# Optimization experiments

Hardware: AMD Instinct MI355X
Metric: run time of the kernel (lower is better)

## Reference

```python
import jax, jax.numpy as jnp
import numpy as np

B, N, C, K = 4, 1024, 384, 10


def _sqdist(a, b):
    # a: [B,P,3], b: [B,M,3] -> [B,P,M] squared euclidean distance
    d = (jnp.sum(a * a, -1)[:, :, None] + jnp.sum(b * b, -1)[:, None, :]
         - 2.0 * jnp.einsum('bpc,bmc->bpm', a, b))
    return jnp.maximum(d, 0.0)


def _gather(points, idx):
    # points: [B,M,C], idx: [B,...] int -> [B,...,C]  (index_points)
    return jax.vmap(lambda p, i: p[i])(points, idx)


def setup_inputs() -> dict:
    key = jax.random.key(0)
    ks = jax.random.split(key, 8)
    def lin(k_, fan_in, fan_out):
        return jax.random.normal(k_, (fan_in, fan_out), jnp.float32) * (1.0 / np.sqrt(fan_in))
    return {
        'q': jax.random.normal(ks[0], (B, N, C), jnp.float32),
        'q_pos': jax.random.normal(ks[1], (B, N, 3), jnp.float32),
        'Wv': lin(ks[2], C, C), 'bv': jnp.zeros((C,), jnp.float32),
        'W1': lin(ks[3], 2 * C, C), 'b1': jnp.zeros((C,), jnp.float32),
        'ln_g': jnp.ones((C,), jnp.float32), 'ln_b': jnp.zeros((C,), jnp.float32),
        'W2': lin(ks[4], C, 3),
        'Wk': lin(ks[5], 2 * C, C), 'bk': jnp.zeros((C,), jnp.float32),
    }


def reference(q, q_pos, Wv, bv, W1, b1, ln_g, ln_b, W2, Wk, bk):
    Bq, Nq, Cq = q.shape
    # 1) KNN of each query among all points (self-attn: v=q, v_pos=q_pos)
    d = _sqdist(q_pos, q_pos)                      # [B,N,N]
    _, idx = jax.lax.top_k(-d, K)                  # [B,N,K] (smallest distances)
    # 2) offset prediction from gathered projected features + query feature
    v_off = q @ Wv + bv                            # [B,N,C]
    off_local_v = _gather(v_off, idx)              # [B,N,K,C]
    qk = jnp.broadcast_to(q[:, :, None, :], (Bq, Nq, K, Cq))
    shift_feat = jnp.concatenate([off_local_v, qk], -1)  # [B,N,K,2C]
    h = shift_feat @ W1 + b1
    mu = jnp.mean(h, -1, keepdims=True)
    var = jnp.var(h, -1, keepdims=True)
    h = (h - mu) / jnp.sqrt(var + 1e-5) * ln_g + ln_b     # LayerNorm
    h = jax.nn.gelu(h, approximate=False)
    offset = jnp.tanh(h @ W2)                      # [B,N,K,3]
    # 3) deformed positions, scaled by half the local bbox extent
    local_v_pos = _gather(q_pos, idx)              # [B,N,K,3]
    scale = (local_v_pos.max(-2) - local_v_pos.min(-2))[:, :, None, :] * 0.5
    shift_pos = (local_v_pos + offset * scale).reshape(Bq, Nq * K, 3)
    # 4) three_nn + three_interpolate (inverse-squared-distance weights)
    d2 = _sqdist(shift_pos, q_pos)                 # [B,NK,N]
    negd, idx3 = jax.lax.top_k(-d2, 3)             # [B,NK,3]
    dist = -negd
    w = 1.0 / (dist + 1e-8)
    w = w / jnp.sum(w, -1, keepdims=True)
    feats3 = _gather(q, idx3)                      # [B,NK,3,C]
    interp = jnp.einsum('bpt,bptc->bpc', w, feats3).reshape(Bq, Nq, K, Cq)
    # 5) graph conv: concat(diff, q) -> Linear -> LeakyReLU(0.2) -> max over K
    feature = jnp.concatenate([interp - qk, qk], -1)      # [B,N,K,2C]
    out = jax.nn.leaky_relu(feature @ Wk + bk, negative_slope=0.2)
    return out.max(-2)                             # [B,N,C]
```

## Files before the change

### kernel.cpp

```cpp
#include <hip/hip_runtime.h>
#include <math.h>

#define BB 4
#define NN 1024
#define CC 384
#define KK 10
#define NKK (NN*KK)

typedef __attribute__((ext_vector_type(8))) short short8v;
typedef __attribute__((ext_vector_type(8))) unsigned short ushort8v;
typedef __attribute__((ext_vector_type(4))) float f32x4;

template <int NA>
__device__ __forceinline__ void wave_sum_arr(float* a) {
  #pragma unroll
  for (int off = 32; off > 0; off >>= 1) {
    float t[NA];
    #pragma unroll
    for (int u = 0; u < NA; ++u) t[u] = __shfl_xor(a[u], off, 64);
    #pragma unroll
    for (int u = 0; u < NA; ++u) a[u] += t[u];
  }
}

__device__ __forceinline__ unsigned short f2bf(float x) {
  unsigned int b = __float_as_uint(x);
  return (unsigned short)((b + 0x7fffu + ((b >> 16) & 1u)) >> 16);
}
__device__ __forceinline__ float bf2f(unsigned short h) {
  return __uint_as_float(((unsigned int)h) << 16);
}

#define NB_CVT  (BB * NN * CC / 1024)
#define NB_PB   (2 * CC * CC / 256)
#define NB_PREP (NB_CVT + NB_PB + 3)
__global__ __launch_bounds__(256) void prep_gemm_kernel(
    const float* __restrict__ q,
    const float* __restrict__ W1, const float* __restrict__ b1,
    const float* __restrict__ bv, const float* __restrict__ bk,
    const float* __restrict__ Wk, const float* __restrict__ Wv,
    unsigned short* __restrict__ qh, unsigned short* __restrict__ ql,
    unsigned short* __restrict__ Wt,
    float* __restrict__ bias_uv, float* __restrict__ bias_pb,
    float* __restrict__ M1p) {
  int blk = blockIdx.x;
  int tid = threadIdx.x;
  if (blk < NB_CVT) {
    int i = (blk * 256 + tid) * 4;
    float4 v = *reinterpret_cast<const float4*>(q + i);
    float x[4] = {v.x, v.y, v.z, v.w};
    #pragma unroll
    for (int j = 0; j < 4; ++j) {
      unsigned short h = f2bf(x[j]);
      qh[i + j] = h;
      ql[i + j] = f2bf(x[j] - bf2f(h));
    }
    return;
  }
  if (blk < NB_CVT + NB_PB) {
    int idx = (blk - NB_CVT) * 256 + tid;
    int n = idx / CC, k = idx % CC;
    float v;
    if (n < CC) v = Wk[(size_t)k * CC + n];
    else        v = Wk[(size_t)CC * CC + k * CC + (n - CC)] - Wk[(size_t)k * CC + (n - CC)];
    Wt[(size_t)n * CC + k] = f2bf(v);
    return;
  }
  if (blk < NB_PREP) {
    int j = (blk - NB_CVT - NB_PB) * 256 + tid;
    if (j >= 2 * CC) return;
    if (j < CC) { bias_uv[j] = 0.f; bias_pb[j] = 0.f; }
    else {
      int c = j - CC;
      float s = b1[c];
      for (int i = 0; i < CC; ++i) s += bv[i] * W1[i * CC + c];
      bias_uv[j] = s;
      bias_pb[j] = bk[c];
    }
    return;
  }
  {
    int r = blk - NB_PREP;
    int bx = r % 3, by = (r / 3) % 3, bz = r / 9;
    __shared__ float As[16][132];
    __shared__ float Bs[16][128];
    int tx = tid & 15, ty = tid >> 4;
    int row0 = by * 128, col0 = bx * 128;
    int k0 = bz * 48;
    float acc[8][8] = {};
    int arow = tid >> 2, akc = (tid & 3) << 2;
    int brow = tid >> 5, bcol = (tid & 31) << 2;
    for (int kt = k0; kt < k0 + 48; kt += 16) {
      #pragma unroll
      for (int h = 0; h < 2; ++h) {
        int rr = arow + 64 * h;
        float4 av = *reinterpret_cast<const float4*>(Wv + (size_t)(row0 + rr) * CC + kt + akc);
        As[akc + 0][rr] = av.x; As[akc + 1][rr] = av.y;
        As[akc + 2][rr] = av.z; As[akc + 3][rr] = av.w;
      }
      #pragma unroll
      for (int h = 0; h < 2; ++h) {
        int rr = brow + 8 * h;
        float4 bv4 = *reinterpret_cast<const float4*>(W1 + (size_t)(kt + rr) * CC + col0 + bcol);
        *reinterpret_cast<float4*>(&Bs[rr][bcol]) = bv4;
      }
      __syncthreads();
      #pragma unroll
      for (int kk = 0; kk < 16; ++kk) {
        float4 a0 = *reinterpret_cast<const float4*>(&As[kk][ty << 2]);
        float4 a1 = *reinterpret_cast<const float4*>(&As[kk][64 + (ty << 2)]);
        float4 b0 = *reinterpret_cast<const float4*>(&Bs[kk][tx << 2]);
        float4 b1 = *reinterpret_cast<const float4*>(&Bs[kk][64 + (tx << 2)]);
        float av_[8] = {a0.x, a0.y, a0.z, a0.w, a1.x, a1.y, a1.z, a1.w};
        float bv_[8] = {b0.x, b0.y, b0.z, b0.w, b1.x, b1.y, b1.z, b1.w};
        #pragma unroll
        for (int i = 0; i < 8; ++i)
          #pragma unroll
          for (int j = 0; j < 8; ++j) acc[i][j] += av_[i] * bv_[j];
      }
      __syncthreads();
    }
    float* Cz = M1p + (size_t)bz * CC * CC;
    #pragma unroll
    for (int i = 0; i < 8; ++i) {
      int row = row0 + (ty << 2) + (i & 3) + ((i & 4) << 4);
      if (row >= CC) continue;
      #pragma unroll
      for (int h = 0; h < 2; ++h) {
        int col = col0 + 64 * h + (tx << 2);
        if (col >= CC) continue;
        float4 rv;
        rv.x = acc[i][4 * h + 0]; rv.y = acc[i][4 * h + 1];
        rv.z = acc[i][4 * h + 2]; rv.w = acc[i][4 * h + 3];
        *reinterpret_cast<float4*>(Cz + (size_t)row * CC + col) = rv;
      }
    }
  }
}

__global__ void pack_uv_split_kernel(const float* __restrict__ M1p, const float* __restrict__ W1,
                                     unsigned short* __restrict__ Buvh,
                                     unsigned short* __restrict__ Buvl) {
  int idx = blockIdx.x * 256 + threadIdx.x;
  int k = idx / (2 * CC), n = idx % (2 * CC);
  float val;
  if (n < CC) {
    float s = 0.f;
    #pragma unroll
    for (int p = 0; p < 8; ++p) s += M1p[(size_t)p * CC * CC + (size_t)k * CC + n];
    val = s;
  } else {
    val = W1[(size_t)(CC + k) * CC + (n - CC)];
  }
  unsigned short h = f2bf(val);
  Buvh[(size_t)n * CC + k] = h;
  Buvl[(size_t)n * CC + k] = f2bf(val - bf2f(h));
}

__global__ __launch_bounds__(256) void gemm_mfma_kernel(
    const unsigned short* __restrict__ qh, const unsigned short* __restrict__ ql,
    const unsigned short* __restrict__ Buvh, const unsigned short* __restrict__ Buvl,
    const unsigned short* __restrict__ Wt,
    float* __restrict__ Cuv, float* __restrict__ Cpb,
    const float* __restrict__ bias_uv, const float* __restrict__ bias_pb) {
  int path = blockIdx.z;
  const unsigned short* Bh = path ? Wt : Buvh;
  float* Cm = path ? Cpb : Cuv;
  const float* bias = path ? bias_pb : bias_uv;
  __shared__ unsigned short Ah[128 * 32], Alo[128 * 32];
  __shared__ unsigned short Bhs[128 * 32], Bls[128 * 32];
  int tid = threadIdx.x;
  int lane = tid & 63, w = tid >> 6;
  int m0 = blockIdx.y * 128, n0 = blockIdx.x * 128;
  f32x4 acc[4][4];
  #pragma unroll
  for (int i = 0; i < 4; ++i)
    #pragma unroll
    for (int j = 0; j < 4; ++j) acc[i][j] = (f32x4){0.f, 0.f, 0.f, 0.f};
  int rl = lane & 15, kg = lane >> 4;
  for (int k0 = 0; k0 < CC; k0 += 32) {
    #pragma unroll
    for (int j = 0; j < 2; ++j) {
      int id = tid + 256 * j;
      int r = id >> 2, s = id & 3;
      int sw = (s ^ (r & 3)) * 8;
      *reinterpret_cast<ushort8v*>(Ah + r * 32 + sw) =
          *reinterpret_cast<const ushort8v*>(qh + (size_t)(m0 + r) * CC + k0 + s * 8);
      *reinterpret_cast<ushort8v*>(Bhs + r * 32 + sw) =
          *reinterpret_cast<const ushort8v*>(Bh + (size_t)(n0 + r) * CC + k0 + s * 8);
      if (!path) {
        *reinterpret_cast<ushort8v*>(Alo + r * 32 + sw) =
            *reinterpret_cast<const ushort8v*>(ql + (size_t)(m0 + r) * CC + k0 + s * 8);
        *reinterpret_cast<ushort8v*>(Bls + r * 32 + sw) =
            *reinterpret_cast<const ushort8v*>(Buvl + (size_t)(n0 + r) * CC + k0 + s * 8);
      }
    }
    __syncthreads();
    short8v afh[4], bfh[4], afl[4], bfl[4];
    #pragma unroll
    for (int f = 0; f < 4; ++f) {
      int ar = (w & 1) * 64 + f * 16 + rl;
      int aof = ar * 32 + (kg ^ (ar & 3)) * 8;
      int br = (w >> 1) * 64 + f * 16 + rl;
      int bof = br * 32 + (kg ^ (br & 3)) * 8;
      afh[f] = *reinterpret_cast<const short8v*>(Ah + aof);
      bfh[f] = *reinterpret_cast<const short8v*>(Bhs + bof);
      if (!path) {
        afl[f] = *reinterpret_cast<const short8v*>(Alo + aof);
        bfl[f] = *reinterpret_cast<const short8v*>(Bls + bof);
      }
    }
    #pragma unroll
    for (int i = 0; i < 4; ++i) {
      #pragma unroll
      for (int j = 0; j < 4; ++j) {
        acc[i][j] = __builtin_amdgcn_mfma_f32_16x16x32_bf16(afh[i], bfh[j], acc[i][j], 0, 0, 0);
        if (!path) {
          acc[i][j] = __builtin_amdgcn_mfma_f32_16x16x32_bf16(afh[i], bfl[j], acc[i][j], 0, 0, 0);
          acc[i][j] = __builtin_amdgcn_mfma_f32_16x16x32_bf16(afl[i], bfh[j], acc[i][j], 0, 0, 0);
        }
      }
    }
    __syncthreads();
  }
  #pragma unroll
  for (int i = 0; i < 4; ++i) {
    #pragma unroll
    for (int j = 0; j < 4; ++j) {
      int col = n0 + (w >> 1) * 64 + j * 16 + rl;
      float bcol_v = bias[col];
      #pragma unroll
      for (int r = 0; r < 4; ++r) {
        int row = m0 + (w & 1) * 64 + i * 16 + kg * 4 + r;
        Cm[(size_t)row * (2 * CC) + col] = acc[i][j][r] + bcol_v;
      }
    }
  }
}

__global__ __launch_bounds__(256) void geo_kernel(
    const float* __restrict__ Cat_uv, const float* __restrict__ lng, const float* __restrict__ lnb,
    const float* __restrict__ W2, const float* __restrict__ q_pos,
    float* __restrict__ shp) {
  int blk = blockIdx.x;
  int b = blk >> 8;
  int ng = blk & 255;
  int tid = threadIdx.x;
  int wave = tid >> 6, lane = tid & 63;
  int n = ng * 4 + wave;
  int bn = b * NN + n;
  __shared__ float4 sp4[NN];

  const float* qp = q_pos + (size_t)b * NN * 3;
  for (int i = tid; i < NN; i += 256) {
    float x = qp[i * 3 + 0], y = qp[i * 3 + 1], z = qp[i * 3 + 2];
    sp4[i] = (float4){x, y, z, x * x + y * y + z * z};
  }
  float Vv[6], lg[6], lb[6], w2a[6], w2b[6], w2c[6];
  const float* Vrow = Cat_uv + (size_t)bn * (2 * CC) + CC;
  #pragma unroll
  for (int i = 0; i < 6; ++i) {
    int c = lane + (i << 6);
    Vv[i] = Vrow[c];
    lg[i] = lng[c]; lb[i] = lnb[c];
    w2a[i] = W2[c * 3 + 0]; w2b[i] = W2[c * 3 + 1]; w2c[i] = W2[c * 3 + 2];
  }
  __syncthreads();

  int nb[KK];
  {
    float4 me = sp4[n];
    float px = me.x, py = me.y, pz = me.z, sp = me.w;
    float bd[KK]; int bi[KK];
    #pragma unroll
    for (int s = 0; s < KK; ++s) { bd[s] = 1e30f; bi[s] = -1; }
    #pragma unroll 4
    for (int j = 0; j < 16; ++j) {
      int m = lane + (j << 6);
      float4 c = sp4[m];
      float dot = fmaf(px, c.x, fmaf(py, c.y, pz * c.z));
      float d = fmaf(-2.f, dot, sp + c.w);
      d = fmaxf(d, 0.f);
      if (d < bd[KK - 1]) {
        bd[KK - 1] = d; bi[KK - 1] = m;
        #pragma unroll
        for (int s = KK - 1; s >= 1; --s) {
          if (bd[s] < bd[s - 1]) {
            float td = bd[s]; bd[s] = bd[s - 1]; bd[s - 1] = td;
            int ti = bi[s]; bi[s] = bi[s - 1]; bi[s - 1] = ti;
          }
        }
      }
    }
    #pragma unroll
    for (int s = 0; s < KK; ++s) {
      float d = bd[0]; int i = bi[0];
      #pragma unroll
      for (int off = 32; off > 0; off >>= 1) {
        float od = __shfl_xor(d, off, 64);
        int oi = __shfl_xor(i, off, 64);
        if (od < d || (od == d && oi < i)) { d = od; i = oi; }
      }
      if (bi[0] == i) {
        #pragma unroll
        for (int u = 0; u < KK - 1; ++u) { bd[u] = bd[u + 1]; bi[u] = bi[u + 1]; }
        bd[KK - 1] = 1e30f; bi[KK - 1] = -1;
      }
      nb[s] = i;
    }
  }

  float sclx, scly, sclz;
  {
    float mxx = -1e30f, mnx = 1e30f, mxy = -1e30f, mny = 1e30f, mxz = -1e30f, mnz = 1e30f;
    #pragma unroll
    for (int k2 = 0; k2 < KK; ++k2) {
      float4 c = sp4[nb[k2]];
      mxx = fmaxf(mxx, c.x); mnx = fminf(mnx, c.x);
      mxy = fmaxf(mxy, c.y); mny = fminf(mny, c.y);
      mxz = fmaxf(mxz, c.z); mnz = fminf(mnz, c.z);
    }
    sclx = (mxx - mnx) * 0.5f; scly = (mxy - mny) * 0.5f; sclz = (mxz - mnz) * 0.5f;
  }

  float ox = 0.f, oy = 0.f, oz = 0.f;
  #pragma unroll
  for (int half = 0; half < 2; ++half) {
    int kb = half * 5;
    float hk[5][6];
    float sum[5];
    #pragma unroll
    for (int kk = 0; kk < 5; ++kk) {
      const float* Urow = Cat_uv + ((size_t)b * NN + nb[kb + kk]) * (2 * CC);
      float s = 0.f;
      #pragma unroll
      for (int i = 0; i < 6; ++i) {
        hk[kk][i] = Urow[lane + (i << 6)] + Vv[i];
        s += hk[kk][i];
      }
      sum[kk] = s;
    }
    wave_sum_arr<5>(sum);
    float mu[5], var[5];
    #pragma unroll
    for (int kk = 0; kk < 5; ++kk) {
      mu[kk] = sum[kk] * (1.0f / CC);
      float v = 0.f;
      #pragma unroll
      for (int i = 0; i < 6; ++i) { float d = hk[kk][i] - mu[kk]; v += d * d; }
      var[kk] = v;
    }
    wave_sum_arr<5>(var);
    float o[15];
    #pragma unroll
    for (int kk = 0; kk < 5; ++kk) {
      float rstd = 1.0f / sqrtf(var[kk] * (1.0f / CC) + 1e-5f);
      float o0 = 0.f, o1 = 0.f, o2 = 0.f;
      #pragma unroll
      for (int i = 0; i < 6; ++i) {
        float x = (hk[kk][i] - mu[kk]) * rstd * lg[i] + lb[i];
        float g = 0.5f * x * (1.0f + erff(x * 0.70710678118654752440f));
        o0 = fmaf(g, w2a[i], o0); o1 = fmaf(g, w2b[i], o1); o2 = fmaf(g, w2c[i], o2);
      }
      o[kk * 3 + 0] = o0; o[kk * 3 + 1] = o1; o[kk * 3 + 2] = o2;
    }
    wave_sum_arr<15>(o);
    #pragma unroll
    for (int kk = 0; kk < 5; ++kk) {
      if (lane == kb + kk) { ox = o[kk * 3 + 0]; oy = o[kk * 3 + 1]; oz = o[kk * 3 + 2]; }
    }
  }
  int myn = 0;
  #pragma unroll
  for (int k = 0; k < KK; ++k) if (lane == k) myn = nb[k];
  if (lane < KK) {
    float4 lv = sp4[myn];
    float* sp = shp + ((size_t)bn * KK + lane) * 3;
    sp[0] = lv.x + tanhf(ox) * sclx;
    sp[1] = lv.y + tanhf(oy) * scly;
    sp[2] = lv.z + tanhf(oz) * sclz;
  }
}

__global__ __launch_bounds__(256) void interp_kernel(
    const float* __restrict__ Cat_pb, const float* __restrict__ q_pos,
    const float* __restrict__ shp, float* __restrict__ out) {
  int bn = blockIdx.x;
  int b = bn >> 10;
  int tid = threadIdx.x;
  int wave = tid >> 6, lane = tid & 63;
  __shared__ float4 sp4[NN];
  __shared__ float s_shp[KK * 3];
  __shared__ float s_w[KK][3];
  __shared__ int s_i[KK][3];

  const float* qp = q_pos + (size_t)b * NN * 3;
  for (int i = tid; i < NN; i += 256) {
    float x = qp[i * 3 + 0], y = qp[i * 3 + 1], z = qp[i * 3 + 2];
    sp4[i] = (float4){x, y, z, x * x + y * y + z * z};
  }
  if (tid < KK * 3) s_shp[tid] = shp[(size_t)bn * KK * 3 + tid];
  __syncthreads();

  int cnt = (wave < 2) ? 3 : 2;
  int pbase = (wave < 2) ? wave * 3 : 6 + (wave - 2) * 2;
  float px[3], py[3], pz[3], ps[3];
  #pragma unroll
  for (int j = 0; j < 3; ++j) {
    int p = pbase + (j < cnt ? j : cnt - 1);
    px[j] = s_shp[p * 3 + 0]; py[j] = s_shp[p * 3 + 1]; pz[j] = s_shp[p * 3 + 2];
    ps[j] = fmaf(px[j], px[j], fmaf(py[j], py[j], pz[j] * pz[j]));
  }
  float d0[3], d1[3], d2[3]; int i0[3], i1[3], i2[3];
  #pragma unroll
  for (int j = 0; j < 3; ++j) { d0[j] = d1[j] = d2[j] = 1e30f; i0[j] = i1[j] = i2[j] = -1; }
  #pragma unroll 4
  for (int it = 0; it < 16; ++it) {
    int m = lane + (it << 6);
    float4 c = sp4[m];
    #pragma unroll
    for (int j = 0; j < 3; ++j) {
      float dot = fmaf(px[j], c.x, fmaf(py[j], c.y, pz[j] * c.z));
      float d = fmaf(-2.f, dot, ps[j] + c.w);
      d = fmaxf(d, 0.f);
      bool c2 = d < d2[j], c1 = d < d1[j], c0 = d < d0[j];
      d2[j] = c1 ? d1[j] : (c2 ? d : d2[j]);  i2[j] = c1 ? i1[j] : (c2 ? m : i2[j]);
      d1[j] = c0 ? d0[j] : (c1 ? d : d1[j]);  i1[j] = c0 ? i0[j] : (c1 ? m : i1[j]);
      d0[j] = c0 ? d : d0[j];                 i0[j] = c0 ? m : i0[j];
    }
  }
  float wd[3][3]; int wi[3][3];
  #pragma unroll
  for (int s = 0; s < 3; ++s) {
    float d[3]; int ii[3];
    #pragma unroll
    for (int j = 0; j < 3; ++j) { d[j] = d0[j]; ii[j] = i0[j]; }
    #pragma unroll
    for (int off = 32; off > 0; off >>= 1) {
      #pragma unroll
      for (int j = 0; j < 3; ++j) {
        float od = __shfl_xor(d[j], off, 64);
        int oi = __shfl_xor(ii[j], off, 64);
        if (od < d[j] || (od == d[j] && oi < ii[j])) { d[j] = od; ii[j] = oi; }
      }
    }
    #pragma unroll
    for (int j = 0; j < 3; ++j) {
      if (i0[j] == ii[j]) {
        d0[j] = d1[j]; i0[j] = i1[j]; d1[j] = d2[j]; i1[j] = i2[j]; d2[j] = 1e30f; i2[j] = -1;
      }
      wd[s][j] = d[j]; wi[s][j] = ii[j];
    }
  }
  if (lane == 0) {
    #pragma unroll
    for (int j = 0; j < 3; ++j) {
      if (j < cnt) {
        float w0 = 1.f / (wd[0][j] + 1e-8f), w1 = 1.f / (wd[1][j] + 1e-8f), w2 = 1.f / (wd[2][j] + 1e-8f);
        float s = w0 + w1 + w2;
        int p = pbase + j;
        s_w[p][0] = w0 / s; s_w[p][1] = w1 / s; s_w[p][2] = w2 / s;
        s_i[p][0] = wi[0][j]; s_i[p][1] = wi[1][j]; s_i[p][2] = wi[2][j];
      }
    }
  }
  __syncthreads();

  const float* Pb = Cat_pb + (size_t)b * NN * (2 * CC);
  const float* BseRow = Cat_pb + (size_t)bn * (2 * CC) + CC;
  for (int c = tid; c < CC; c += 256) {
    float base = BseRow[c];
    float best = -1e30f;
    #pragma unroll
    for (int k = 0; k < KK; ++k) {
      float acc = base;
      #pragma unroll
      for (int tt = 0; tt < 3; ++tt)
        acc = fmaf(s_w[k][tt], Pb[(size_t)s_i[k][tt] * (2 * CC) + c], acc);
      acc = acc >= 0.f ? acc : 0.2f * acc;
      best = fmaxf(best, acc);
    }
    out[(size_t)bn * CC + c] = best;
  }
}

extern "C" void kernel_launch(void* const* d_in, const int* in_sizes, int n_in,
                              void* d_out, int out_size, void* d_ws, size_t ws_size,
                              hipStream_t stream) {
  (void)in_sizes; (void)n_in; (void)out_size; (void)ws_size;
  const float* q    = (const float*)d_in[0];
  const float* qpos = (const float*)d_in[1];
  const float* Wv   = (const float*)d_in[2];
  const float* bv   = (const float*)d_in[3];
  const float* W1   = (const float*)d_in[4];
  const float* b1   = (const float*)d_in[5];
  const float* lng  = (const float*)d_in[6];
  const float* lnb  = (const float*)d_in[7];
  const float* W2   = (const float*)d_in[8];
  const float* Wk   = (const float*)d_in[9];
  const float* bk   = (const float*)d_in[10];
  float* out = (float*)d_out;

  float* ws = (float*)d_ws;
  float* Cat_uv = ws; ws += (size_t)BB * NN * 2 * CC;
  float* Cat_pb = ws; ws += (size_t)BB * NN * 2 * CC;
  float* M1p = Cat_pb;
  float* bias_uv = ws; ws += 2 * CC;
  float* bias_pb = ws; ws += 2 * CC;
  float* shp = ws; ws += (size_t)BB * NKK * 3;
  unsigned short* qh = (unsigned short*)ws;  ws += (size_t)BB * NN * CC / 2;
  unsigned short* ql = (unsigned short*)ws;  ws += (size_t)BB * NN * CC / 2;
  unsigned short* Wt = (unsigned short*)ws;  ws += (size_t)2 * CC * CC / 2;
  unsigned short* Buvh = (unsigned short*)ws; ws += (size_t)2 * CC * CC / 2;
  unsigned short* Buvl = (unsigned short*)ws; ws += (size_t)2 * CC * CC / 2;

  prep_gemm_kernel<<<dim3(NB_PREP + 72), dim3(256), 0, stream>>>(
      q, W1, b1, bv, bk, Wk, Wv, qh, ql, Wt, bias_uv, bias_pb, M1p);
  pack_uv_split_kernel<<<dim3(CC * 2 * CC / 256), dim3(256), 0, stream>>>(M1p, W1, Buvh, Buvl);
  gemm_mfma_kernel<<<dim3(2 * CC / 128, BB * NN / 128, 2), dim3(256), 0, stream>>>(
      qh, ql, Buvh, Buvl, Wt, Cat_uv, Cat_pb, bias_uv, bias_pb);
  geo_kernel<<<dim3(BB * NN / 4), dim3(256), 0, stream>>>(
      Cat_uv, lng, lnb, W2, qpos, shp);
  interp_kernel<<<dim3(BB * NN), dim3(256), 0, stream>>>(
      Cat_pb, qpos, shp, out);
}
```

Baseline: 161.2 us.

## Split geo kernel into separate KNN and per-neighbor MLP kernels

The fused geometry kernel is split into a KNN kernel, which writes neighbor indices, neighbor positions and bbox scales to a workspace buffer, and an MLP kernel. In the MLP kernel each wave handles five of the ten neighbors instead of one wave doing all ten in two serial halves. This doubles the wave-level parallelism for the LayerNorm/GELU/offset MLP and shortens the per-wave dependency chain. In exchange it adds a kernel launch and a global round-trip for indices and metadata. The KNN could also run while the GEMM runs, but the code keeps everything on one stream.

```diff
diff --git a/kernel.cpp b/kernel.cpp
--- a/kernel.cpp
+++ b/kernel.cpp
@@ -238,10 +238,8 @@
   }
 }
 
-__global__ __launch_bounds__(256) void geo_kernel(
-    const float* __restrict__ Cat_uv, const float* __restrict__ lng, const float* __restrict__ lnb,
-    const float* __restrict__ W2, const float* __restrict__ q_pos,
-    float* __restrict__ shp) {
+__global__ __launch_bounds__(256) void knn_kernel(
+    const float* __restrict__ q_pos, int* __restrict__ idxk, float* __restrict__ meta) {
   int blk = blockIdx.x;
   int b = blk >> 8;
   int ng = blk & 255;
@@ -255,15 +253,6 @@
   for (int i = tid; i < NN; i += 256) {
     float x = qp[i * 3 + 0], y = qp[i * 3 + 1], z = qp[i * 3 + 2];
     sp4[i] = (float4){x, y, z, x * x + y * y + z * z};
-  }
-  float Vv[6], lg[6], lb[6], w2a[6], w2b[6], w2c[6];
-  const float* Vrow = Cat_uv + (size_t)bn * (2 * CC) + CC;
-  #pragma unroll
-  for (int i = 0; i < 6; ++i) {
-    int c = lane + (i << 6);
-    Vv[i] = Vrow[c];
-    lg[i] = lng[c]; lb[i] = lnb[c];
-    w2a[i] = W2[c * 3 + 0]; w2b[i] = W2[c * 3 + 1]; w2c[i] = W2[c * 3 + 2];
   }
   __syncthreads();
 
@@ -323,62 +312,95 @@
     sclx = (mxx - mnx) * 0.5f; scly = (mxy - mny) * 0.5f; sclz = (mxz - mnz) * 0.5f;
   }
 
+  int myn = 0;
+  #pragma unroll
+  for (int k = 0; k < KK; ++k) if (lane == k) myn = nb[k];
+  float* mrow = meta + (size_t)bn * 36;
+  if (lane < KK) {
+    idxk[(size_t)bn * KK + lane] = myn;
+    float4 c = sp4[myn];
+    mrow[lane * 3 + 0] = c.x;
+    mrow[lane * 3 + 1] = c.y;
+    mrow[lane * 3 + 2] = c.z;
+  }
+  if (lane == 0) { mrow[30] = sclx; mrow[31] = scly; mrow[32] = sclz; }
+}
+
+__global__ __launch_bounds__(256) void mlp_kernel(
+    const float* __restrict__ Cat_uv, const float* __restrict__ lng, const float* __restrict__ lnb,
+    const float* __restrict__ W2, const int* __restrict__ idxk, const float* __restrict__ meta,
+    float* __restrict__ shp) {
+  int tid = threadIdx.x;
+  int wave = tid >> 6, lane = tid & 63;
+  int bn = blockIdx.x * 2 + (wave >> 1);
+  int b = bn >> 10;
+  int kb = (wave & 1) * 5;
+
+  int nb5[5];
+  #pragma unroll
+  for (int kk = 0; kk < 5; ++kk) nb5[kk] = idxk[(size_t)bn * KK + kb + kk];
+
+  float Vv[6], lg[6], lb[6], w2a[6], w2b[6], w2c[6];
+  const float* Vrow = Cat_uv + (size_t)bn * (2 * CC) + CC;
+  #pragma unroll
+  for (int i = 0; i < 6; ++i) {
+    int c = lane + (i << 6);
+    Vv[i] = Vrow[c];
+    lg[i] = lng[c]; lb[i] = lnb[c];
+    w2a[i] = W2[c * 3 + 0]; w2b[i] = W2[c * 3 + 1]; w2c[i] = W2[c * 3 + 2];
+  }
+
+  float hk[5][6];
+  float sum[5];
+  #pragma unroll
+  for (int kk = 0; kk < 5; ++kk) {
+    const float* Urow = Cat_uv + ((size_t)b * NN + nb5[kk]) * (2 * CC);
+    float s = 0.f;
+    #pragma unroll
+    for (int i = 0; i < 6; ++i) {
+      hk[kk][i] = Urow[lane + (i << 6)] + Vv[i];
+      s += hk[kk][i];
+    }
+    sum[kk] = s;
+  }
+  wave_sum_arr<5>(sum);
+  float mu[5], var[5];
+  #pragma unroll
+  for (int kk = 0; kk < 5; ++kk) {
+    mu[kk] = sum[kk] * (1.0f / CC);
+    float v = 0.f;
+    #pragma unroll
+    for (int i = 0; i < 6; ++i) { float d = hk[kk][i] - mu[kk]; v += d * d; }
+    var[kk] = v;
+  }
+  wave_sum_arr<5>(var);
+  float o[15];
+  #pragma unroll
+  for (int kk = 0; kk < 5; ++kk) {
+    float rstd = 1.0f / sqrtf(var[kk] * (1.0f / CC) + 1e-5f);
+    float o0 = 0.f, o1 = 0.f, o2 = 0.f;
+    #pragma unroll
+    for (int i = 0; i < 6; ++i) {
+      float x = (hk[kk][i] - mu[kk]) * rstd * lg[i] + lb[i];
+      float g = 0.5f * x * (1.0f + erff(x * 0.70710678118654752440f));
+      o0 = fmaf(g, w2a[i], o0); o1 = fmaf(g, w2b[i], o1); o2 = fmaf(g, w2c[i], o2);
+    }
+    o[kk * 3 + 0] = o0; o[kk * 3 + 1] = o1; o[kk * 3 + 2] = o2;
+  }
+  wave_sum_arr<15>(o);
   float ox = 0.f, oy = 0.f, oz = 0.f;
   #pragma unroll
-  for (int half = 0; half < 2; ++half) {
-    int kb = half * 5;
-    float hk[5][6];
-    float sum[5];
-    #pragma unroll
-    for (int kk = 0; kk < 5; ++kk) {
-      const float* Urow = Cat_uv + ((size_t)b * NN + nb[kb + kk]) * (2 * CC);
-      float s = 0.f;
-      #pragma unroll
-      for (int i = 0; i < 6; ++i) {
-        hk[kk][i] = Urow[lane + (i << 6)] + Vv[i];
-        s += hk[kk][i];
-      }
-      sum[kk] = s;
-    }
-    wave_sum_arr<5>(sum);
-    float mu[5], var[5];
-    #pragma unroll
-    for (int kk = 0; kk < 5; ++kk) {
-      mu[kk] = sum[kk] * (1.0f / CC);
-      float v = 0.f;
-      #pragma unroll
-      for (int i = 0; i < 6; ++i) { float d = hk[kk][i] - mu[kk]; v += d * d; }
-      var[kk] = v;
-    }
-    wave_sum_arr<5>(var);
-    float o[15];
-    #pragma unroll
-    for (int kk = 0; kk < 5; ++kk) {
-      float rstd = 1.0f / sqrtf(var[kk] * (1.0f / CC) + 1e-5f);
-      float o0 = 0.f, o1 = 0.f, o2 = 0.f;
-      #pragma unroll
-      for (int i = 0; i < 6; ++i) {
-        float x = (hk[kk][i] - mu[kk]) * rstd * lg[i] + lb[i];
-        float g = 0.5f * x * (1.0f + erff(x * 0.70710678118654752440f));
-        o0 = fmaf(g, w2a[i], o0); o1 = fmaf(g, w2b[i], o1); o2 = fmaf(g, w2c[i], o2);
-      }
-      o[kk * 3 + 0] = o0; o[kk * 3 + 1] = o1; o[kk * 3 + 2] = o2;
-    }
-    wave_sum_arr<15>(o);
-    #pragma unroll
-    for (int kk = 0; kk < 5; ++kk) {
-      if (lane == kb + kk) { ox = o[kk * 3 + 0]; oy = o[kk * 3 + 1]; oz = o[kk * 3 + 2]; }
-    }
-  }
-  int myn = 0;
-  #pragma unroll
-  for (int k = 0; k < KK; ++k) if (lane == k) myn = nb[k];
-  if (lane < KK) {
-    float4 lv = sp4[myn];
+  for (int kk = 0; kk < 5; ++kk) {
+    if (lane == kb + kk) { ox = o[kk * 3 + 0]; oy = o[kk * 3 + 1]; oz = o[kk * 3 + 2]; }
+  }
+  if (lane >= kb && lane < kb + 5) {
+    const float* mrow = meta + (size_t)bn * 36;
+    float lvx = mrow[lane * 3 + 0], lvy = mrow[lane * 3 + 1], lvz = mrow[lane * 3 + 2];
+    float sclx = mrow[30], scly = mrow[31], sclz = mrow[32];
     float* sp = shp + ((size_t)bn * KK + lane) * 3;
-    sp[0] = lv.x + tanhf(ox) * sclx;
-    sp[1] = lv.y + tanhf(oy) * scly;
-    sp[2] = lv.z + tanhf(oz) * sclz;
+    sp[0] = lvx + tanhf(ox) * sclx;
+    sp[1] = lvy + tanhf(oy) * scly;
+    sp[2] = lvz + tanhf(oz) * sclz;
   }
 }
 
@@ -508,19 +530,22 @@
   float* bias_uv = ws; ws += 2 * CC;
   float* bias_pb = ws; ws += 2 * CC;
   float* shp = ws; ws += (size_t)BB * NKK * 3;
+  float* meta = ws; ws += (size_t)BB * NN * 36;
   unsigned short* qh = (unsigned short*)ws;  ws += (size_t)BB * NN * CC / 2;
   unsigned short* ql = (unsigned short*)ws;  ws += (size_t)BB * NN * CC / 2;
   unsigned short* Wt = (unsigned short*)ws;  ws += (size_t)2 * CC * CC / 2;
   unsigned short* Buvh = (unsigned short*)ws; ws += (size_t)2 * CC * CC / 2;
   unsigned short* Buvl = (unsigned short*)ws; ws += (size_t)2 * CC * CC / 2;
+  int* idxk = (int*)ws;
 
   prep_gemm_kernel<<<dim3(NB_PREP + 72), dim3(256), 0, stream>>>(
       q, W1, b1, bv, bk, Wk, Wv, qh, ql, Wt, bias_uv, bias_pb, M1p);
   pack_uv_split_kernel<<<dim3(CC * 2 * CC / 256), dim3(256), 0, stream>>>(M1p, W1, Buvh, Buvl);
   gemm_mfma_kernel<<<dim3(2 * CC / 128, BB * NN / 128, 2), dim3(256), 0, stream>>>(
       qh, ql, Buvh, Buvl, Wt, Cat_uv, Cat_pb, bias_uv, bias_pb);
-  geo_kernel<<<dim3(BB * NN / 4), dim3(256), 0, stream>>>(
-      Cat_uv, lng, lnb, W2, qpos, shp);
+  knn_kernel<<<dim3(BB * NN / 4), dim3(256), 0, stream>>>(qpos, idxk, meta);
+  mlp_kernel<<<dim3(BB * NN / 2), dim3(256), 0, stream>>>(
+      Cat_uv, lng, lnb, W2, idxk, meta, shp);
   interp_kernel<<<dim3(BB * NN), dim3(256), 0, stream>>>(
       Cat_pb, qpos, shp, out);
 }
```

New measurement: 148.6 us. 7.8% less time.
